# Kernel optimization log

Hardware: AMD Instinct MI355X
Metric: run time of the kernel (lower is better)

The kernel has to match this reference:

```python
import jax, jax.numpy as jnp
import numpy as np

LS = 64                      # latent_scaling
TYPES = [8, 1, 1]            # Pyr, SST, VIP widths
DEPTHS = [1, 1, 1]           # L4, L23, L5
B, T = 64, 256
I = 2 * 1 * len(TYPES) * len(DEPTHS)          # 18
AREA = sum(TYPES) * sum(DEPTHS) * LS          # 1920 per area
H = 2 * AREA                                  # 3840


def _build_mask():
    """Block-structured Bernoulli sign mask over 2 areas x (3 layers x 3 types).

    Mirrors the BB* buffers of celltypeRNN: within-area blocks drawn
    Bernoulli(p) with sign +1 for Pyr sources, -1 for SST/VIP sources;
    cross-area blocks zero.
    """
    rng = np.random.default_rng(0)
    # population order per area: (L4,Pyr),(L4,SST),(L4,VIP),(L23,...),(L5,...)
    sizes = [DEPTHS[l] * TYPES[t] * LS for l in range(3) for t in range(3)]
    offs = np.concatenate([[0], np.cumsum(sizes)])
    n_pop = 9
    # connection probability table P[src, dst] (from the source's pvals;
    # unspecified pairs default to 0.05)
    P = np.full((n_pop, n_pop), 0.05)
    # self blocks (diagonal): L4 [.1,.01,.03], L23 [.06,.05,.01], L5 [.04,.03,.03]
    diag = [0.10, 0.01, 0.03, 0.06, 0.05, 0.01, 0.04, 0.03, 0.03]
    for i, p in enumerate(diag):
        P[i, i] = p
    # L4Pyr (idx 0) -> others
    for dst, p in [(1, .04), (4, .04), (7, .03), (2, .00), (5, .02), (8, .11), (3, .07), (6, .00)]:
        P[0, dst] = p
    # L4SST (idx 1) -> others
    for dst, p in [(0, .22), (3, .33), (6, .08), (2, .22), (5, .21), (8, .07), (4, .05), (7, .04)]:
        P[1, dst] = p
    # L4VIP (idx 2) -> Pyr
    P[2, 0] = 0.0
    P[2, 3] = 0.0
    sign = np.array([+1.0, -1.0, -1.0] * 3)  # Pyr +, SST -, VIP -
    mask = np.zeros((H, H), dtype=np.float32)
    for area in range(2):           # V1, LM (within-area connectivity only)
        base = area * AREA
        for s in range(n_pop):
            for d in range(n_pop):
                r0, r1 = base + offs[d], base + offs[d + 1]
                c0, c1 = base + offs[s], base + offs[s + 1]
                blk = (rng.random((r1 - r0, c1 - c0)) < P[s, d]).astype(np.float32)
                mask[r0:r1, c0:c1] = blk * sign[s]
    return jnp.asarray(mask)


def setup_inputs() -> dict:
    key = jax.random.key(0)
    kx, kwi, kbi, kwh, kbh = jax.random.split(key, 5)
    s = 1.0 / np.sqrt(H)
    return {
        "x": jax.random.normal(kx, (B, T, I), jnp.float32),
        "W_ih": jax.random.uniform(kwi, (H, I), jnp.float32, -s, s),
        "b_ih": jax.random.uniform(kbi, (H,), jnp.float32, -s, s),
        "W_hh": jax.random.uniform(kwh, (H, H), jnp.float32, -s, s),
        "b_hh": jax.random.uniform(kbh, (H,), jnp.float32, -s, s),
        "mask": _build_mask(),
    }


def reference(x, W_ih, b_ih, W_hh, b_hh, mask):
    # cell-type connectivity mask applied to the recurrent weights
    Wm = W_hh * mask                              # [H, H]
    # precompute input projection for all timesteps: [B, T, H]
    xp = jnp.einsum("bti,hi->bth", x, W_ih) + b_ih + b_hh
    h0 = jnp.zeros((x.shape[0], Wm.shape[0]), x.dtype)

    def step(h, xp_t):                            # h: [B, H], xp_t: [B, H]
        h = jax.nn.relu(xp_t + h @ Wm.T)
        return h, h

    _, hs = jax.lax.scan(step, h0, jnp.swapaxes(xp, 0, 1))  # [T, B, H]
    return jnp.swapaxes(hs, 0, 1)                            # [B, T, H]
```

## Files before the change

kernel.cpp:

```cpp
#include <hip/hip_runtime.h>
#include <stdint.h>
#include <stddef.h>

#define HH 3840
#define AH 1920
#define NI 18
#define NT 256
#define NBATCH 64
#define KMAX 224
#define JSLOT 28
#define NRW 120
#define NB 8
#define NGROUP 16
#define NBLK_G 16
#define NBLOCKS 256
#define NTHREADS 1024
#define COLS 1920
#define COLT 1938
#define HNEW_PAD 9

#define ENT_BYTES ((size_t)HH * KMAX * 4)
#define CNT_BYTES ((size_t)HH * 4)
#define XT2_BYTES ((size_t)NT * NI * NBATCH * 2)
#define HT_HALF   ((size_t)NGROUP * AH * NB)
#define HT_BYTES  (2 * HT_HALF * 2)
#define FLAG_ELEMS ((size_t)NGROUP * NBLK_G * 32)
#define PC_ELEMS  16

#define SLAB_B    (COLT * 16)
#define OFF_HNEW  (2 * SLAB_B)
#define HNEW_B    (2 * NRW * HNEW_PAD * 4)
#define SMEM_USED (OFF_HNEW + HNEW_B)
#define SMEM_ALLOC 83968

#define AS1 __attribute__((address_space(1)))
#define AS3 __attribute__((address_space(3)))

typedef unsigned long long u64;

__device__ __forceinline__ float lo16(uint32_t u) {
    union { uint16_t q; _Float16 h; } c; c.q = (uint16_t)u; return (float)c.h;
}
__device__ __forceinline__ uint16_t f2h_bits(float f) {
    union { _Float16 h; uint16_t u; } c; c.h = (_Float16)f; return c.u;
}
__device__ __forceinline__ uint32_t pkrtz(float x, float y) {
    typedef __fp16 h2 __attribute__((ext_vector_type(2)));
    union { h2 h; uint32_t u; } c; c.h = __builtin_amdgcn_cvt_pkrtz(x, y); return c.u;
}
__device__ __forceinline__ void gll16(const void* g, void* l) {
    __builtin_amdgcn_global_load_lds((const AS1 uint32_t*)g, (AS3 uint32_t*)l, 16, 0, 0);
}
__device__ __forceinline__ void astore(u64* p, u64 v) {
    __hip_atomic_store(p, v, __ATOMIC_RELAXED, __HIP_MEMORY_SCOPE_AGENT);
}
__device__ __forceinline__ uint32_t sel8(const uint32_t v[8], int b) {
    uint32_t x = v[0];
    #pragma unroll
    for (int i = 1; i < 8; ++i) x = (b == i) ? v[i] : x;
    return x;
}
__device__ __forceinline__ u64 sel8_64(const u64 v[8], int b) {
    u64 x = v[0];
    #pragma unroll
    for (int i = 1; i < 8; ++i) x = (b == i) ? v[i] : x;
    return x;
}
#define SWZ(v, pat) __uint_as_float(__builtin_amdgcn_ds_swizzle(__float_as_uint(v), pat))
#define DPA(c, ctrl) c += __uint_as_float(__builtin_amdgcn_mov_dpp(__float_as_uint(c), ctrl, 0xF, 0xF, true))
#define FMIX_LO(acc, h2, w) asm("v_fma_mix_f32 %0, %1, %2, %0 op_sel:[0,0,0] op_sel_hi:[1,0,0]" : "+v"(acc) : "v"(h2), "v"(w))
#define FMIX_HI(acc, h2, w) asm("v_fma_mix_f32 %0, %1, %2, %0 op_sel:[1,0,0] op_sel_hi:[1,0,0]" : "+v"(acc) : "v"(h2), "v"(w))

__global__ void init_ws_kernel(uint32_t* __restrict__ flg, uint32_t* __restrict__ ht0) {
    size_t i = (size_t)blockIdx.x * blockDim.x + threadIdx.x;
    if (i < FLAG_ELEMS + PC_ELEMS) flg[i] = 0;
    if (i < HT_HALF / 2) ht0[i] = 0;
}

__global__ void build_ell_kernel(const float* __restrict__ Whh, const float* __restrict__ mask,
                                 const float* __restrict__ Wih,
                                 uint32_t* __restrict__ ent, uint32_t* __restrict__ cnt) {
    int gw = (int)((blockIdx.x * blockDim.x + threadIdx.x) >> 6);
    int lane = threadIdx.x & 63;
    if (gw >= HH) return;
    const int d = gw;
    const int area = (d >= AH) ? 1 : 0;
    const float* mrow = mask + (size_t)d * HH + (size_t)area * AH;
    const float* wrow = Whh + (size_t)d * HH + (size_t)area * AH;
    uint32_t* erow = ent + (size_t)d * KMAX;
    const u64 below = ((u64)1 << lane) - 1;

    uint32_t sz[8] = {0, 0, 0, 0, 0, 0, 0, 0};
    for (int c0 = 0; c0 <= AH; c0 += 64) {
        bool isx = (c0 == AH);
        bool pred;
        if (isx) pred = (lane < NI);
        else     pred = (mrow[c0 + lane] != 0.0f);
        int b = lane & 7;
        #pragma unroll
        for (int bb = 0; bb < 8; ++bb)
            sz[bb] += (uint32_t)__popcll(__ballot(pred && (b == bb)));
    }
    uint32_t run[8] = {0, 0, 0, 0, 0, 0, 0, 0};
    for (int c0 = 0; c0 <= AH; c0 += 64) {
        bool isx = (c0 == AH);
        int col; bool pred; float wval;
        if (isx) {
            col = COLS + lane; pred = (lane < NI);
            wval = pred ? Wih[(size_t)d * NI + lane] : 0.0f;
        } else {
            col = c0 + lane;
            float m = mrow[col];
            pred = (m != 0.0f);
            wval = pred ? wrow[col] * m : 0.0f;
        }
        int b = lane & 7;
        u64 bal[8];
        #pragma unroll
        for (int bb = 0; bb < 8; ++bb) bal[bb] = __ballot(pred && (b == bb));
        if (pred) {
            uint32_t k = sel8(run, b) + (uint32_t)__popcll(sel8_64(bal, b) & below);
            uint32_t rank = k;
            #pragma unroll
            for (int bb = 0; bb < 8; ++bb) {
                uint32_t cap = (bb < b) ? (k + 1) : k;
                uint32_t add = (sz[bb] < cap) ? sz[bb] : cap;
                rank += (bb == b) ? 0u : add;
            }
            if (rank < KMAX) erow[rank] = ((uint32_t)col << 16) | (uint32_t)f2h_bits(wval);
        }
        #pragma unroll
        for (int bb = 0; bb < 8; ++bb) run[bb] += (uint32_t)__popcll(bal[bb]);
    }
    uint32_t tot = sz[0] + sz[1] + sz[2] + sz[3] + sz[4] + sz[5] + sz[6] + sz[7];
    if (lane == 0) cnt[d] = (tot < KMAX) ? tot : KMAX;
}

__global__ void xt_kernel(const float* __restrict__ x, uint16_t* __restrict__ xT2) {
    int i = blockIdx.x * blockDim.x + threadIdx.x;
    if (i >= NT * NI * NBATCH) return;
    int b = i % NBATCH;
    int rest = i / NBATCH;
    int ii = rest % NI;
    int t = rest / NI;
    xT2[i] = f2h_bits(x[((size_t)b * NT + t) * NI + ii]);
}

__global__ __launch_bounds__(NTHREADS, 4) void rnn_kernel(
    const uint32_t* __restrict__ ent, const uint32_t* __restrict__ cnt,
    const uint16_t* __restrict__ xT2, uint16_t* __restrict__ hT,
    uint32_t* __restrict__ flg,
    const float* __restrict__ bih, const float* __restrict__ bhh,
    float* __restrict__ out)
{
    extern __shared__ char smem[];
    uint4* slab = (uint4*)smem;
    float* hnew = (float*)(smem + OFF_HNEW);

    const int tid = threadIdx.x;
    const int G = blockIdx.x & 15, role = blockIdx.x >> 4;
    const int a = G >> 3, g = G & 7;
    const int row0 = role * NRW;
    const size_t mySlot = ((size_t)G * NBLK_G + role) * 32;

    const int wv = tid >> 6, lane = tid & 63;
    const int ro = lane >> 3;
    const int kq = lane & 7;
    const int r  = wv * 8 + ro;

    float wj[JSLOT];
    int   aj[JSLOT];
    float biasr = 0.f;
    int wm = 0;
    if (wv < 15) {
        const int gRow = a * AH + row0 + r;
        const int n = (int)cnt[gRow];
        biasr = bih[gRow] + bhh[gRow];
        int jmax = (n > kq) ? ((n - kq + 7) >> 3) : 0;
        const uint32_t* ep = ent + (size_t)gRow * KMAX;
        #pragma unroll
        for (int j = 0; j < JSLOT; ++j) {
            uint32_t e = (j < jmax) ? ep[kq + 8 * j] : 0u;
            aj[j] = (int)((e >> 16) * 16);
            wj[j] = (j < jmax) ? lo16(e) : 0.0f;
        }
        wm = jmax;
        #pragma unroll
        for (int s = 1; s < 64; s <<= 1) {
            int ov = __shfl_xor(wm, s, 64);
            wm = (ov > wm) ? ov : wm;
        }
    }

    for (int t = 0; t < NT; ++t) {
        const int cur = t & 1, nxt = cur ^ 1;
        if (wv == 0 && lane < NI)
            gll16(xT2 + ((size_t)t * NI + lane) * NBATCH + g * NB,
                  &slab[cur * COLT + COLS + lane]);
        if (wv > 0 || t == 0) {
            const int p = (role + wv) & 15;
            if (t > 0) {
                const uint32_t* sl = flg + ((size_t)G * NBLK_G + p) * 32;
                int guard = 0;
                while (__hip_atomic_load(sl, __ATOMIC_RELAXED, __HIP_MEMORY_SCOPE_AGENT)
                       < (uint32_t)t && ++guard < (1 << 15))
                    __builtin_amdgcn_s_sleep(1);
            }
            const uint4* sp = (const uint4*)(hT + (size_t)cur * HT_HALF
                                             + ((size_t)G * AH + p * NRW) * NB);
            const int l2 = (lane < 56) ? (64 + lane) : lane;
            uint4 v0, v1;
            asm volatile("global_load_dwordx4 %0, %2, off sc0 sc1\n\t"
                         "global_load_dwordx4 %1, %3, off sc0 sc1\n\t"
                         "s_waitcnt vmcnt(0)"
                         : "=&v"(v0), "=&v"(v1)
                         : "v"(sp + lane), "v"(sp + l2)
                         : "memory");
            uint4* dst = slab + cur * COLT + p * NRW;
            dst[lane] = v0;
            dst[l2] = v1;
        }
        __syncthreads();

        if (wv == 15 && t > 0) {
            const float* hp = hnew + ((t - 1) & 1) * NRW * HNEW_PAD;
            for (int i = lane; i < NB * NRW; i += 64) {
                int bb = i / NRW, d = i - bb * NRW;
                out[(((size_t)(g * NB + bb)) * NT + (t - 1)) * HH + (size_t)a * AH + row0 + d]
                    = hp[d * HNEW_PAD + bb];
            }
        }

        if (wv < 15) {
            const char* sb = (const char*)(slab + cur * COLT);
            float c0 = 0.f, c1 = 0.f, c2 = 0.f, c3 = 0.f, c4 = 0.f, c5 = 0.f, c6 = 0.f, c7 = 0.f;
            #pragma unroll
            for (int j = 0; j < JSLOT; ++j) {
                if (j >= wm) break;
                const uint4 hv = *(const uint4*)(sb + aj[j]);
                const float wf = wj[j];
                FMIX_LO(c0, hv.x, wf); FMIX_HI(c1, hv.x, wf);
                FMIX_LO(c2, hv.y, wf); FMIX_HI(c3, hv.y, wf);
                FMIX_LO(c4, hv.z, wf); FMIX_HI(c5, hv.z, wf);
                FMIX_LO(c6, hv.w, wf); FMIX_HI(c7, hv.w, wf);
            }
            c0 += SWZ(c0, 0x101F); c1 += SWZ(c1, 0x101F); c2 += SWZ(c2, 0x101F); c3 += SWZ(c3, 0x101F);
            c4 += SWZ(c4, 0x101F); c5 += SWZ(c5, 0x101F); c6 += SWZ(c6, 0x101F); c7 += SWZ(c7, 0x101F);
            DPA(c0, 0x4E); DPA(c1, 0x4E); DPA(c2, 0x4E); DPA(c3, 0x4E);
            DPA(c4, 0x4E); DPA(c5, 0x4E); DPA(c6, 0x4E); DPA(c7, 0x4E);
            DPA(c0, 0xB1); DPA(c1, 0xB1); DPA(c2, 0xB1); DPA(c3, 0xB1);
            DPA(c4, 0xB1); DPA(c5, 0xB1); DPA(c6, 0xB1); DPA(c7, 0xB1);
            if (kq == 0) {
                float h0 = fmaxf(c0 + biasr, 0.f), h1 = fmaxf(c1 + biasr, 0.f);
                float h2 = fmaxf(c2 + biasr, 0.f), h3 = fmaxf(c3 + biasr, 0.f);
                float h4 = fmaxf(c4 + biasr, 0.f), h5 = fmaxf(c5 + biasr, 0.f);
                float h6 = fmaxf(c6 + biasr, 0.f), h7 = fmaxf(c7 + biasr, 0.f);
                uint4 pk;
                pk.x = pkrtz(h0, h1); pk.y = pkrtz(h2, h3);
                pk.z = pkrtz(h4, h5); pk.w = pkrtz(h6, h7);
                u64* dst8 = (u64*)(hT + (size_t)nxt * HT_HALF
                                   + ((size_t)G * AH + row0 + r) * NB);
                astore(dst8,     ((u64)pk.y << 32) | pk.x);
                astore(dst8 + 1, ((u64)pk.w << 32) | pk.z);
                slab[nxt * COLT + row0 + r] = pk;
                float* hp = hnew + cur * NRW * HNEW_PAD + r * HNEW_PAD;
                hp[0] = h0; hp[1] = h1; hp[2] = h2; hp[3] = h3;
                hp[4] = h4; hp[5] = h5; hp[6] = h6; hp[7] = h7;
            }
        }
        __syncthreads();

        if (tid == 0)
            __hip_atomic_store(flg + mySlot, (uint32_t)(t + 1), __ATOMIC_RELAXED,
                               __HIP_MEMORY_SCOPE_AGENT);
    }
    {
        const float* hp = hnew + ((NT - 1) & 1) * NRW * HNEW_PAD;
        for (int i = tid; i < NB * NRW; i += NTHREADS) {
            int bb = i / NRW, d = i - bb * NRW;
            out[(((size_t)(g * NB + bb)) * NT + (NT - 1)) * HH + (size_t)a * AH + row0 + d]
                = hp[d * HNEW_PAD + bb];
        }
    }
}

extern "C" void kernel_launch(void* const* d_in, const int* in_sizes, int n_in,
                              void* d_out, int out_size, void* d_ws, size_t ws_size,
                              hipStream_t stream)
{
    const float* x    = (const float*)d_in[0];
    const float* Wih  = (const float*)d_in[1];
    const float* bih  = (const float*)d_in[2];
    const float* Whh  = (const float*)d_in[3];
    const float* bhh  = (const float*)d_in[4];
    const float* mask = (const float*)d_in[5];
    float* out = (float*)d_out;

    char* ws = (char*)d_ws;
    uint32_t* ent = (uint32_t*)(ws);
    uint32_t* cnt = (uint32_t*)(ws + ENT_BYTES);
    uint16_t* xT2 = (uint16_t*)(ws + ENT_BYTES + CNT_BYTES);
    uint16_t* hT  = (uint16_t*)(ws + ENT_BYTES + CNT_BYTES + XT2_BYTES);
    uint32_t* flg = (uint32_t*)(ws + ENT_BYTES + CNT_BYTES + XT2_BYTES + HT_BYTES);

    init_ws_kernel<<<512, 256, 0, stream>>>(flg, (uint32_t*)hT);
    build_ell_kernel<<<(HH * 64 + 255) / 256, 256, 0, stream>>>(Whh, mask, Wih, ent, cnt);
    xt_kernel<<<(NT * NI * NBATCH + 255) / 256, 256, 0, stream>>>(x, xT2);

    hipFuncSetAttribute((const void*)rnn_kernel,
                        hipFuncAttributeMaxDynamicSharedMemorySize, SMEM_ALLOC);

    void* args[] = {(void*)&ent, (void*)&cnt, (void*)&xT2, (void*)&hT, (void*)&flg,
                    (void*)&bih, (void*)&bhh, (void*)&out};
    hipLaunchCooperativeKernel((const void*)rnn_kernel, dim3(NBLOCKS), dim3(NTHREADS),
                               args, SMEM_ALLOC, stream);
}
```

Baseline: 1.250 ms.

## Permute hidden rows by degree to balance sparse work across waves and blocks

Adds a degree count and a rank-based permutation so hidden units are sorted by nonzero count and dealt round-robin across the 16 row-blocks, with 8-row groups of similar degree sharing a wave. The ELL build, bias lookup and output scatter are remapped through the permutation. The aim is to cut the per-wave loop trip count (max over 64 lanes) and balance blocks, since Pyr rows have many more nonzeros than SST/VIP rows. Costs are extra preprocessing kernels, including an O(AH^2) rank computation, and scattered rather than contiguous output writes.

```diff
diff --git a/kernel.cpp b/kernel.cpp
--- a/kernel.cpp
+++ b/kernel.cpp
@@ -26,11 +26,13 @@
 #define HT_BYTES  (2 * HT_HALF * 2)
 #define FLAG_ELEMS ((size_t)NGROUP * NBLK_G * 32)
 #define PC_ELEMS  16
+#define PERM_BYTES ((size_t)HH * 4)
 
 #define SLAB_B    (COLT * 16)
 #define OFF_HNEW  (2 * SLAB_B)
 #define HNEW_B    (2 * NRW * HNEW_PAD * 4)
-#define SMEM_USED (OFF_HNEW + HNEW_B)
+#define OFF_IPERM (OFF_HNEW + HNEW_B)
+#define SMEM_USED (OFF_IPERM + NRW * 4)
 #define SMEM_ALLOC 83968
 
 #define AS1 __attribute__((address_space(1)))
@@ -77,26 +79,59 @@
     if (i < HT_HALF / 2) ht0[i] = 0;
 }
 
+__global__ void deg_kernel(const float* __restrict__ mask, uint32_t* __restrict__ deg) {
+    int gw = (int)((blockIdx.x * blockDim.x + threadIdx.x) >> 6);
+    int lane = threadIdx.x & 63;
+    if (gw >= HH) return;
+    int area = (gw >= AH) ? 1 : 0;
+    const float* mrow = mask + (size_t)gw * HH + (size_t)area * AH;
+    uint32_t n = 0;
+    for (int c0 = 0; c0 < AH; c0 += 64)
+        n += (uint32_t)__popcll(__ballot(mrow[c0 + lane] != 0.0f));
+    if (lane == 0) deg[gw] = n + NI;
+}
+
+__global__ void perm_kernel(const uint32_t* __restrict__ deg,
+                            uint32_t* __restrict__ posA, uint32_t* __restrict__ invA) {
+    int d = blockIdx.x * blockDim.x + threadIdx.x;
+    if (d >= HH) return;
+    int area = (d >= AH) ? 1 : 0;
+    int i = d - area * AH;
+    const uint32_t* db = deg + (size_t)area * AH;
+    uint32_t di = db[i];
+    uint32_t rank = 0;
+    for (int j = 0; j < AH; ++j) {
+        uint32_t dj = db[j];
+        rank += (dj > di || (dj == di && j < i)) ? 1u : 0u;
+    }
+    uint32_t chunk = rank >> 3, o = rank & 7;
+    uint32_t pos = (chunk & 15) * NRW + (chunk >> 4) * 8 + o;
+    posA[d] = pos;
+    invA[(size_t)area * AH + pos] = (uint32_t)i;
+}
+
 __global__ void build_ell_kernel(const float* __restrict__ Whh, const float* __restrict__ mask,
                                  const float* __restrict__ Wih,
+                                 const uint32_t* __restrict__ posA, const uint32_t* __restrict__ invA,
                                  uint32_t* __restrict__ ent, uint32_t* __restrict__ cnt) {
     int gw = (int)((blockIdx.x * blockDim.x + threadIdx.x) >> 6);
     int lane = threadIdx.x & 63;
     if (gw >= HH) return;
-    const int d = gw;
-    const int area = (d >= AH) ? 1 : 0;
-    const float* mrow = mask + (size_t)d * HH + (size_t)area * AH;
-    const float* wrow = Whh + (size_t)d * HH + (size_t)area * AH;
-    uint32_t* erow = ent + (size_t)d * KMAX;
+    const int area = (gw >= AH) ? 1 : 0;
+    const int ol = (int)invA[gw];
+    const size_t og = (size_t)area * AH + ol;
+    const float* mrow = mask + og * HH + (size_t)area * AH;
+    const float* wrow = Whh + og * HH + (size_t)area * AH;
+    const uint32_t* pA = posA + (size_t)area * AH;
+    uint32_t* erow = ent + (size_t)gw * KMAX;
     const u64 below = ((u64)1 << lane) - 1;
 
     uint32_t sz[8] = {0, 0, 0, 0, 0, 0, 0, 0};
     for (int c0 = 0; c0 <= AH; c0 += 64) {
         bool isx = (c0 == AH);
-        bool pred;
-        if (isx) pred = (lane < NI);
-        else     pred = (mrow[c0 + lane] != 0.0f);
-        int b = lane & 7;
+        bool pred; int b;
+        if (isx) { pred = (lane < NI); b = lane & 7; }
+        else     { pred = (mrow[c0 + lane] != 0.0f); b = (int)(pA[c0 + lane] & 7); }
         #pragma unroll
         for (int bb = 0; bb < 8; ++bb)
             sz[bb] += (uint32_t)__popcll(__ballot(pred && (b == bb)));
@@ -104,17 +139,17 @@
     uint32_t run[8] = {0, 0, 0, 0, 0, 0, 0, 0};
     for (int c0 = 0; c0 <= AH; c0 += 64) {
         bool isx = (c0 == AH);
-        int col; bool pred; float wval;
+        int col; bool pred; float wval; int b;
         if (isx) {
-            col = COLS + lane; pred = (lane < NI);
-            wval = pred ? Wih[(size_t)d * NI + lane] : 0.0f;
+            col = COLS + lane; pred = (lane < NI); b = lane & 7;
+            wval = pred ? Wih[og * NI + lane] : 0.0f;
         } else {
-            col = c0 + lane;
-            float m = mrow[col];
+            float m = mrow[c0 + lane];
             pred = (m != 0.0f);
-            wval = pred ? wrow[col] * m : 0.0f;
-        }
-        int b = lane & 7;
+            col = (int)pA[c0 + lane];
+            b = col & 7;
+            wval = pred ? wrow[c0 + lane] * m : 0.0f;
+        }
         u64 bal[8];
         #pragma unroll
         for (int bb = 0; bb < 8; ++bb) bal[bb] = __ballot(pred && (b == bb));
@@ -133,7 +168,7 @@
         for (int bb = 0; bb < 8; ++bb) run[bb] += (uint32_t)__popcll(bal[bb]);
     }
     uint32_t tot = sz[0] + sz[1] + sz[2] + sz[3] + sz[4] + sz[5] + sz[6] + sz[7];
-    if (lane == 0) cnt[d] = (tot < KMAX) ? tot : KMAX;
+    if (lane == 0) cnt[gw] = (tot < KMAX) ? tot : KMAX;
 }
 
 __global__ void xt_kernel(const float* __restrict__ x, uint16_t* __restrict__ xT2) {
@@ -149,13 +184,14 @@
 __global__ __launch_bounds__(NTHREADS, 4) void rnn_kernel(
     const uint32_t* __restrict__ ent, const uint32_t* __restrict__ cnt,
     const uint16_t* __restrict__ xT2, uint16_t* __restrict__ hT,
-    uint32_t* __restrict__ flg,
+    uint32_t* __restrict__ flg, const uint32_t* __restrict__ invA,
     const float* __restrict__ bih, const float* __restrict__ bhh,
     float* __restrict__ out)
 {
     extern __shared__ char smem[];
     uint4* slab = (uint4*)smem;
     float* hnew = (float*)(smem + OFF_HNEW);
+    uint32_t* iperm = (uint32_t*)(smem + OFF_IPERM);
 
     const int tid = threadIdx.x;
     const int G = blockIdx.x & 15, role = blockIdx.x >> 4;
@@ -167,6 +203,9 @@
     const int ro = lane >> 3;
     const int kq = lane & 7;
     const int r  = wv * 8 + ro;
+
+    for (int i = tid; i < NRW; i += NTHREADS)
+        iperm[i] = invA[(size_t)a * AH + row0 + i];
 
     float wj[JSLOT];
     int   aj[JSLOT];
@@ -174,8 +213,9 @@
     int wm = 0;
     if (wv < 15) {
         const int gRow = a * AH + row0 + r;
+        const int ol = (int)invA[gRow];
         const int n = (int)cnt[gRow];
-        biasr = bih[gRow] + bhh[gRow];
+        biasr = bih[a * AH + ol] + bhh[a * AH + ol];
         int jmax = (n > kq) ? ((n - kq + 7) >> 3) : 0;
         const uint32_t* ep = ent + (size_t)gRow * KMAX;
         #pragma unroll
@@ -226,7 +266,7 @@
             const float* hp = hnew + ((t - 1) & 1) * NRW * HNEW_PAD;
             for (int i = lane; i < NB * NRW; i += 64) {
                 int bb = i / NRW, d = i - bb * NRW;
-                out[(((size_t)(g * NB + bb)) * NT + (t - 1)) * HH + (size_t)a * AH + row0 + d]
+                out[(((size_t)(g * NB + bb)) * NT + (t - 1)) * HH + (size_t)a * AH + iperm[d]]
                     = hp[d * HNEW_PAD + bb];
             }
         }
@@ -278,7 +318,7 @@
         const float* hp = hnew + ((NT - 1) & 1) * NRW * HNEW_PAD;
         for (int i = tid; i < NB * NRW; i += NTHREADS) {
             int bb = i / NRW, d = i - bb * NRW;
-            out[(((size_t)(g * NB + bb)) * NT + (NT - 1)) * HH + (size_t)a * AH + row0 + d]
+            out[(((size_t)(g * NB + bb)) * NT + (NT - 1)) * HH + (size_t)a * AH + iperm[d]]
                 = hp[d * HNEW_PAD + bb];
         }
     }
@@ -302,16 +342,23 @@
     uint16_t* xT2 = (uint16_t*)(ws + ENT_BYTES + CNT_BYTES);
     uint16_t* hT  = (uint16_t*)(ws + ENT_BYTES + CNT_BYTES + XT2_BYTES);
     uint32_t* flg = (uint32_t*)(ws + ENT_BYTES + CNT_BYTES + XT2_BYTES + HT_BYTES);
+    char* ptail   = ws + ENT_BYTES + CNT_BYTES + XT2_BYTES + HT_BYTES
+                    + (FLAG_ELEMS + PC_ELEMS) * 4;
+    uint32_t* posA = (uint32_t*)(ptail);
+    uint32_t* invA = (uint32_t*)(ptail + PERM_BYTES);
+    uint32_t* degA = (uint32_t*)(ptail + 2 * PERM_BYTES);
 
     init_ws_kernel<<<512, 256, 0, stream>>>(flg, (uint32_t*)hT);
-    build_ell_kernel<<<(HH * 64 + 255) / 256, 256, 0, stream>>>(Whh, mask, Wih, ent, cnt);
+    deg_kernel<<<(HH * 64 + 255) / 256, 256, 0, stream>>>(mask, degA);
+    perm_kernel<<<(HH + 255) / 256, 256, 0, stream>>>(degA, posA, invA);
+    build_ell_kernel<<<(HH * 64 + 255) / 256, 256, 0, stream>>>(Whh, mask, Wih, posA, invA, ent, cnt);
     xt_kernel<<<(NT * NI * NBATCH + 255) / 256, 256, 0, stream>>>(x, xT2);
 
     hipFuncSetAttribute((const void*)rnn_kernel,
                         hipFuncAttributeMaxDynamicSharedMemorySize, SMEM_ALLOC);
 
     void* args[] = {(void*)&ent, (void*)&cnt, (void*)&xT2, (void*)&hT, (void*)&flg,
-                    (void*)&bih, (void*)&bhh, (void*)&out};
+                    (void*)&invA, (void*)&bih, (void*)&bhh, (void*)&out};
     hipLaunchCooperativeKernel((const void*)rnn_kernel, dim3(NBLOCKS), dim3(NTHREADS),
                                args, SMEM_ALLOC, stream);
 }
```

After: 1.136 ms. 1.1x faster.
